# Kernel tuning notes

Hardware: AMD Instinct MI355X
Metric: run time of the kernel (lower is better)

## Reference

```python
import jax, jax.numpy as jnp
import numpy as np

N = 100_000      # num_nodes
E = 1_600_000    # num_edges (avg degree 16)
D = 64           # embedding_dim
L = 3            # num_layers


def setup_inputs() -> dict:
    key = jax.random.key(0)
    k1, k2 = jax.random.split(key)
    edge_index = jax.random.randint(k1, (2, E), 0, N, dtype=jnp.int64)
    edge_weight = jnp.ones((E,), jnp.float32)
    # nn.init.normal_(std=0.1)
    embedding = 0.1 * jax.random.normal(k2, (N, D), dtype=jnp.float32)
    return {"embedding": embedding, "edge_weight": edge_weight, "edge_index": edge_index}


def reference(embedding, edge_weight, edge_index):
    n = embedding.shape[0]
    self_idx = jnp.arange(n, dtype=edge_index.dtype)
    # add_self_loops: append (i, i) with weight 1 (PyG default fill_value)
    row = jnp.concatenate([edge_index[0], self_idx])  # source j
    col = jnp.concatenate([edge_index[1], self_idx])  # target i
    ew = jnp.concatenate([edge_weight, jnp.ones((n,), embedding.dtype)])
    # degree() counts occurrences of row (unweighted)
    deg = jax.ops.segment_sum(jnp.ones_like(ew), row, num_segments=n)
    deg_inv_sqrt = jnp.where(deg > 0, jax.lax.rsqrt(deg), 0.0)
    norm = deg_inv_sqrt[row] * ew * deg_inv_sqrt[col]  # [E+N]

    x = embedding
    acc = embedding  # running sum of layer-0..L embeddings
    for _ in range(L):
        # gather from source, scale, scatter-add to target (dropout off in eval)
        msg = norm[:, None] * x[row]                       # [E+N, D]
        x = jax.ops.segment_sum(msg, col, num_segments=n)  # [N, D]
        acc = acc + x
    return acc / (L + 1)
```

## Files before the change

### kernel.cpp

```cpp
#include <hip/hip_runtime.h>
#include <stdint.h>

#define DIM 64
#define BINS2 50000
#define RANGES 2
#define NSLICE 64
#define TBH 1024
#define SCAN_TILE 1024

__device__ __forceinline__ unsigned bf16rne(float f) {
    unsigned u = __float_as_uint(f);
    return (u + 0x7FFFu + ((u >> 16) & 1u)) >> 16;
}
__device__ __forceinline__ unsigned pack2(float lo, float hi) {
    return bf16rne(lo) | (bf16rne(hi) << 16);
}
#define UNPK(u, lo, hi) { lo = __uint_as_float((u) << 16); hi = __uint_as_float((u) & 0xFFFF0000u); }

__global__ void __launch_bounds__(TBH)
hist_kernel(const int* __restrict__ src, const int* __restrict__ dst,
            unsigned short* __restrict__ partialsA, unsigned short* __restrict__ partialsB,
            unsigned short* __restrict__ lrank, int E, int N, int Es) {
    __shared__ unsigned h32[BINS2 / 2];
    const int b = blockIdx.x;
    const int kind = b / (RANGES * NSLICE);
    const int rs = b % (RANGES * NSLICE);
    const int r = rs / NSLICE, s = rs % NSLICE;
    const int base = r * BINS2;
    const int hi = min(base + BINS2, N);
    const int nbw = (hi - base + 1) >> 1;
    for (int j = threadIdx.x; j < nbw; j += TBH) h32[j] = 0;
    __syncthreads();
    const int e0 = s * Es, e1 = min(e0 + Es, E);
    if (kind == 0) {
#pragma unroll 4
        for (int i = e0 + threadIdx.x; i < e1; i += TBH) {
            unsigned j = (unsigned)(dst[i] - base);
            if (j < (unsigned)BINS2) {
                const unsigned sh = (j & 1) * 16;
                unsigned old = atomicAdd(&h32[j >> 1], 1u << sh);
                lrank[i] = (unsigned short)((old >> sh) & 0xFFFFu);
            }
        }
    } else {
#pragma unroll 4
        for (int i = e0 + threadIdx.x; i < e1; i += TBH) {
            unsigned j = (unsigned)(src[i] - base);
            if (j < (unsigned)BINS2) atomicAdd(&h32[j >> 1], 1u << ((j & 1) * 16));
        }
    }
    __syncthreads();
    unsigned* part = (unsigned*)((kind ? partialsB : partialsA) + (size_t)s * N + base);
    for (int j = threadIdx.x; j < nbw; j += TBH) part[j] = h32[j];
}

__global__ void __launch_bounds__(256)
merge_kernel(unsigned short* __restrict__ partialsA, const unsigned short* __restrict__ partialsB,
             int* __restrict__ indeg, float* __restrict__ dis, int N) {
    const int i = blockIdx.x * blockDim.x + threadIdx.x;
    if (i >= N) return;
    int run = 0;
    for (int s = 0; s < NSLICE; ++s) {
        int v = partialsA[(size_t)s * N + i];
        partialsA[(size_t)s * N + i] = (unsigned short)run;
        run += v;
    }
    indeg[i] = run;
    int od = 0;
    for (int s = 0; s < NSLICE; ++s) od += partialsB[(size_t)s * N + i];
    dis[i] = rsqrtf((float)od + 1.0f);
}


__global__ void __launch_bounds__(256)
scan_partial(const int* __restrict__ indeg, int* __restrict__ partial, int n) {
    __shared__ int wsum[4];
    const int tid = threadIdx.x;
    const int base = blockIdx.x * SCAN_TILE + tid * 4;
    int s = 0;
    if (base + 3 < n) {
        int4 v = *(const int4*)(indeg + base);
        s = v.x + v.y + v.z + v.w;
    } else {
        for (int i = 0; i < 4; ++i) if (base + i < n) s += indeg[base + i];
    }
    for (int off = 32; off > 0; off >>= 1) s += __shfl_down(s, off, 64);
    const int lane = tid & 63, wid = tid >> 6;
    if (lane == 0) wsum[wid] = s;
    __syncthreads();
    if (tid == 0) partial[blockIdx.x] = wsum[0] + wsum[1] + wsum[2] + wsum[3];
}

__global__ void scan_blocksums(int* __restrict__ partial, int* __restrict__ offsets,
                               int nblocks, int n) {
    __shared__ int buf[1024];
    const int t = threadIdx.x;
    int v = (t < nblocks) ? partial[t] : 0;
    buf[t] = v;
    __syncthreads();
    for (int off = 1; off < 1024; off <<= 1) {
        int add = (t >= off) ? buf[t - off] : 0;
        __syncthreads();
        buf[t] += add;
        __syncthreads();
    }
    if (t < nblocks) partial[t] = buf[t] - v;
    if (t == 1023) offsets[n] = buf[1023];
}

__global__ void __launch_bounds__(256)
scan_final(const int* __restrict__ indeg, const int* __restrict__ partial,
           int* __restrict__ offsets, int n) {
    __shared__ int wpre[4];
    const int tid = threadIdx.x;
    const int base = blockIdx.x * SCAN_TILE + tid * 4;
    int v0 = 0, v1 = 0, v2 = 0, v3 = 0;
    if (base + 3 < n) {
        int4 v = *(const int4*)(indeg + base);
        v0 = v.x; v1 = v.y; v2 = v.z; v3 = v.w;
    } else {
        if (base + 0 < n) v0 = indeg[base + 0];
        if (base + 1 < n) v1 = indeg[base + 1];
        if (base + 2 < n) v2 = indeg[base + 2];
        if (base + 3 < n) v3 = indeg[base + 3];
    }
    const int s = v0 + v1 + v2 + v3;
    int inc = s;
    const int lane = tid & 63, wid = tid >> 6;
    for (int off = 1; off < 64; off <<= 1) {
        int t = __shfl_up(inc, off, 64);
        if (lane >= off) inc += t;
    }
    if (lane == 63) wpre[wid] = inc;
    __syncthreads();
    if (tid == 0) {
        int r = 0;
        for (int w = 0; w < 4; ++w) { int t = wpre[w]; wpre[w] = r; r += t; }
    }
    __syncthreads();
    int run = (inc - s) + wpre[wid] + partial[blockIdx.x];
    if (base + 0 < n) { offsets[base + 0] = run; run += v0; }
    if (base + 1 < n) { offsets[base + 1] = run; run += v1; }
    if (base + 2 < n) { offsets[base + 2] = run; run += v2; }
    if (base + 3 < n) { offsets[base + 3] = run; run += v3; }
}

__global__ void __launch_bounds__(256)
fill_kernel(const int* __restrict__ src, const int* __restrict__ dst,
            const float* __restrict__ ew, const float* __restrict__ dis,
            const int* __restrict__ offsets, const unsigned short* __restrict__ sliceoff,
            const unsigned short* __restrict__ lrank, int2* __restrict__ csr,
            int E, int N, int Es) {
    const int i0 = (blockIdx.x * blockDim.x + threadIdx.x) * 4;
    if (i0 + 3 < E) {
        int4   ss = *(const int4*)(src + i0);
        int4   tt = *(const int4*)(dst + i0);
        float4 ww = *(const float4*)(ew + i0);
        ushort4 lr = *(const ushort4*)(lrank + i0);
#define DO(K, SF, TF, WF, LF) { int sE = (i0 + K) / Es; \
        int slot = offsets[TF] + sliceoff[(size_t)sE * N + TF] + (int)(LF); \
        csr[slot] = make_int2(SF, __float_as_int(dis[SF] * (WF) * dis[TF])); }
        DO(0, ss.x, tt.x, ww.x, lr.x)
        DO(1, ss.y, tt.y, ww.y, lr.y)
        DO(2, ss.z, tt.z, ww.z, lr.z)
        DO(3, ss.w, tt.w, ww.w, lr.w)
#undef DO
    } else {
        for (int i = i0; i < E; ++i) {
            int sE = i / Es;
            int t = dst[i], sc = src[i];
            float w = dis[sc] * ew[i] * dis[t];
            int slot = offsets[t] + sliceoff[(size_t)sE * N + t] + (int)lrank[i];
            csr[slot] = make_int2(sc, __float_as_int(w));
        }
    }
}

__global__ void __launch_bounds__(256)
conv_kernel(const float4* __restrict__ in4, uint4* __restrict__ outb, int n8) {
    int i = blockIdx.x * blockDim.x + threadIdx.x;
    if (i >= n8) return;
    float4 a = in4[2 * i], b = in4[2 * i + 1];
    uint4 o;
    o.x = pack2(a.x, a.y); o.y = pack2(a.z, a.w);
    o.z = pack2(b.x, b.y); o.w = pack2(b.z, b.w);
    outb[i] = o;
}

__global__ void __launch_bounds__(256)
prop_kernel(const uint4* __restrict__ xg, const float4* __restrict__ selfF,
            uint4* __restrict__ xstore,
            const int* __restrict__ offsets, const int2* __restrict__ csr,
            const float* __restrict__ dis, int n) {
    const int lane = threadIdx.x & 63;
    const int fl  = lane & 7;
    const int sub = lane >> 3;
    const int wave = blockIdx.x * (blockDim.x >> 6) + (threadIdx.x >> 6);
    const int node = wave * 8 + sub;
    if (node >= n) return;

    const int beg = offsets[node];
    const int end = offsets[node + 1];
    const float d = dis[node];
    const float dd = d * d;

    float a0, a1, a2, a3, a4, a5, a6, a7;
    if (selfF) {
        float4 s0 = selfF[node * 16 + fl * 2];
        float4 s1 = selfF[node * 16 + fl * 2 + 1];
        a0 = dd * s0.x; a1 = dd * s0.y; a2 = dd * s0.z; a3 = dd * s0.w;
        a4 = dd * s1.x; a5 = dd * s1.y; a6 = dd * s1.z; a7 = dd * s1.w;
    } else {
        uint4 q = xg[(size_t)node * 8 + fl];
        float l, h;
        UNPK(q.x, l, h) a0 = dd * l; a1 = dd * h;
        UNPK(q.y, l, h) a2 = dd * l; a3 = dd * h;
        UNPK(q.z, l, h) a4 = dd * l; a5 = dd * h;
        UNPK(q.w, l, h) a6 = dd * l; a7 = dd * h;
    }

#define EDGE(E, Q) { float w_ = __int_as_float((E).y); float l, h; \
    UNPK((Q).x, l, h) a0 = fmaf(w_, l, a0); a1 = fmaf(w_, h, a1); \
    UNPK((Q).y, l, h) a2 = fmaf(w_, l, a2); a3 = fmaf(w_, h, a3); \
    UNPK((Q).z, l, h) a4 = fmaf(w_, l, a4); a5 = fmaf(w_, h, a5); \
    UNPK((Q).w, l, h) a6 = fmaf(w_, l, a6); a7 = fmaf(w_, h, a7); }

    int p = beg;
    for (; p + 8 <= end; p += 8) {
        int2 e0 = csr[p + 0], e1 = csr[p + 1], e2 = csr[p + 2], e3 = csr[p + 3];
        int2 e4 = csr[p + 4], e5 = csr[p + 5], e6 = csr[p + 6], e7 = csr[p + 7];
        uint4 q0 = xg[(size_t)e0.x * 8 + fl];
        uint4 q1 = xg[(size_t)e1.x * 8 + fl];
        uint4 q2 = xg[(size_t)e2.x * 8 + fl];
        uint4 q3 = xg[(size_t)e3.x * 8 + fl];
        uint4 q4 = xg[(size_t)e4.x * 8 + fl];
        uint4 q5 = xg[(size_t)e5.x * 8 + fl];
        uint4 q6 = xg[(size_t)e6.x * 8 + fl];
        uint4 q7 = xg[(size_t)e7.x * 8 + fl];
        EDGE(e0, q0) EDGE(e1, q1) EDGE(e2, q2) EDGE(e3, q3)
        EDGE(e4, q4) EDGE(e5, q5) EDGE(e6, q6) EDGE(e7, q7)
    }
    for (; p + 4 <= end; p += 4) {
        int2 e0 = csr[p + 0], e1 = csr[p + 1], e2 = csr[p + 2], e3 = csr[p + 3];
        uint4 q0 = xg[(size_t)e0.x * 8 + fl];
        uint4 q1 = xg[(size_t)e1.x * 8 + fl];
        uint4 q2 = xg[(size_t)e2.x * 8 + fl];
        uint4 q3 = xg[(size_t)e3.x * 8 + fl];
        EDGE(e0, q0) EDGE(e1, q1) EDGE(e2, q2) EDGE(e3, q3)
    }
    for (; p < end; ++p) {
        int2 e = csr[p];
        uint4 q = xg[(size_t)e.x * 8 + fl];
        EDGE(e, q)
    }
#undef EDGE

    uint4 o;
    o.x = pack2(a0, a1); o.y = pack2(a2, a3);
    o.z = pack2(a4, a5); o.w = pack2(a6, a7);
    xstore[(size_t)node * 8 + fl] = o;
}

__global__ void __launch_bounds__(256)
combine_kernel(const float4* __restrict__ emb4, const uint4* __restrict__ xa,
               const uint4* __restrict__ xb, const uint4* __restrict__ xc,
               float4* __restrict__ out4, int n8) {
    int i = blockIdx.x * blockDim.x + threadIdx.x;
    if (i >= n8) return;
    float4 e0 = emb4[2 * i], e1 = emb4[2 * i + 1];
    uint4 qa = xa[i], qb = xb[i], qc = xc[i];
    float r[8] = { e0.x, e0.y, e0.z, e0.w, e1.x, e1.y, e1.z, e1.w };
    float l, h;
    UNPK(qa.x, l, h) r[0] += l; r[1] += h;
    UNPK(qa.y, l, h) r[2] += l; r[3] += h;
    UNPK(qa.z, l, h) r[4] += l; r[5] += h;
    UNPK(qa.w, l, h) r[6] += l; r[7] += h;
    UNPK(qb.x, l, h) r[0] += l; r[1] += h;
    UNPK(qb.y, l, h) r[2] += l; r[3] += h;
    UNPK(qb.z, l, h) r[4] += l; r[5] += h;
    UNPK(qb.w, l, h) r[6] += l; r[7] += h;
    UNPK(qc.x, l, h) r[0] += l; r[1] += h;
    UNPK(qc.y, l, h) r[2] += l; r[3] += h;
    UNPK(qc.z, l, h) r[4] += l; r[5] += h;
    UNPK(qc.w, l, h) r[6] += l; r[7] += h;
    out4[2 * i]     = make_float4(0.25f * r[0], 0.25f * r[1], 0.25f * r[2], 0.25f * r[3]);
    out4[2 * i + 1] = make_float4(0.25f * r[4], 0.25f * r[5], 0.25f * r[6], 0.25f * r[7]);
}


extern "C" void kernel_launch(void* const* d_in, const int* in_sizes, int n_in,
                              void* d_out, int out_size, void* d_ws, size_t ws_size,
                              hipStream_t stream) {
    const float* emb = (const float*)d_in[0];
    const float* ew  = (const float*)d_in[1];
    const int*   ei  = (const int*)d_in[2];
    const int E = in_sizes[2] / 2;
    const int N = in_sizes[0] / DIM;
    const int* src = ei;
    const int* dst = ei + E;
    float* out = (float*)d_out;

    const int Es = (E + NSLICE - 1) / NSLICE;
    const int nscan = (N + SCAN_TILE - 1) / SCAN_TILE;

    char* w = (char*)d_ws;
    size_t partSz = ((size_t)NSLICE * N * 2 + 255) & ~(size_t)255;
    size_t xSz    = ((size_t)N * DIM * 2 + 255) & ~(size_t)255;
    size_t uSz    = (partSz > xSz) ? partSz : xSz;
    unsigned short* partialsA = (unsigned short*)w;
    uint4* xc = (uint4*)w; w += uSz;
    unsigned short* partialsB = (unsigned short*)w;
    uint4* xb = (uint4*)w; w += uSz;
    unsigned short* lrank = (unsigned short*)w; w += (size_t)E * 2;
    int* indeg   = (int*)w;  w += (size_t)N * 4;
    int* offsets = (int*)w;  w += (size_t)(N + 1) * 4;
    float* dis   = (float*)w; w += (size_t)N * 4;
    int* partial = (int*)w;  w += (size_t)1024 * 4;
    w = (char*)(((uintptr_t)w + 255) & ~(uintptr_t)255);
    int2* csr    = (int2*)w; w += (size_t)E * 8;
    w = (char*)(((uintptr_t)w + 255) & ~(uintptr_t)255);
    uint4* x0c   = (uint4*)w; w += xSz;
    uint4* xa    = (uint4*)w; w += xSz;

    const int TB = 256;
    hist_kernel<<<2 * RANGES * NSLICE, TBH, 0, stream>>>(src, dst, partialsA, partialsB,
                                                         lrank, E, N, Es);
    merge_kernel<<<(N + TB - 1) / TB, TB, 0, stream>>>(partialsA, partialsB,
                                                       indeg, dis, N);
    scan_partial<<<nscan, TB, 0, stream>>>(indeg, partial, N);
    scan_blocksums<<<1, 1024, 0, stream>>>(partial, offsets, nscan, N);
    scan_final<<<nscan, TB, 0, stream>>>(indeg, partial, offsets, N);
    const int e4 = (E + 3) / 4;
    fill_kernel<<<(e4 + TB - 1) / TB, TB, 0, stream>>>(src, dst, ew, dis, offsets,
                                                       partialsA, lrank, csr, E, N, Es);
    const int n8 = N * DIM / 8;
    conv_kernel<<<(n8 + TB - 1) / TB, TB, 0, stream>>>((const float4*)emb, x0c, n8);

    dim3 grid((N + 31) / 32), block(TB);
    prop_kernel<<<grid, block, 0, stream>>>(x0c, (const float4*)emb, xa,
                                            offsets, csr, dis, N);
    prop_kernel<<<grid, block, 0, stream>>>(xa, nullptr, xb,
                                            offsets, csr, dis, N);
    prop_kernel<<<grid, block, 0, stream>>>(xb, nullptr, xc,
                                            offsets, csr, dis, N);
    combine_kernel<<<(n8 + TB - 1) / TB, TB, 0, stream>>>((const float4*)emb, xa, xb, xc,
                                                          (float4*)out, n8);
}
```

Before: 284.8 us.

## Replace sliced shared-memory histogram CSR build with global atomics and two-pass bucketed placement

Replaces the 64-slice shared-memory histogram plus per-slice prefix merge with global-atomic degree counting. The CSR is now built by partitioning edges into 128-node buckets via block-local histograms and global cursors, then placing them within each bucket using shared-memory atomics. The aim is to avoid the large NSLICE×N partial arrays and the scattered per-edge slot writes. The cost is an extra staging pass over E records, contended global atomics, and an in-bucket edge order that is no longer deterministic. That order changes the floating-point summation order, and the source index must fit in 20 bits.

```diff
diff --git a/kernel.cpp b/kernel.cpp
--- a/kernel.cpp
+++ b/kernel.cpp
@@ -2,10 +2,10 @@
 #include <stdint.h>
 
 #define DIM 64
-#define BINS2 50000
-#define RANGES 2
-#define NSLICE 64
-#define TBH 1024
+#define GB 128
+#define GSH 7
+#define CH 8192
+#define TB1 512
 #define SCAN_TILE 1024
 
 __device__ __forceinline__ unsigned bf16rne(float f) {
@@ -17,58 +17,23 @@
 }
 #define UNPK(u, lo, hi) { lo = __uint_as_float((u) << 16); hi = __uint_as_float((u) & 0xFFFF0000u); }
 
-__global__ void __launch_bounds__(TBH)
-hist_kernel(const int* __restrict__ src, const int* __restrict__ dst,
-            unsigned short* __restrict__ partialsA, unsigned short* __restrict__ partialsB,
-            unsigned short* __restrict__ lrank, int E, int N, int Es) {
-    __shared__ unsigned h32[BINS2 / 2];
-    const int b = blockIdx.x;
-    const int kind = b / (RANGES * NSLICE);
-    const int rs = b % (RANGES * NSLICE);
-    const int r = rs / NSLICE, s = rs % NSLICE;
-    const int base = r * BINS2;
-    const int hi = min(base + BINS2, N);
-    const int nbw = (hi - base + 1) >> 1;
-    for (int j = threadIdx.x; j < nbw; j += TBH) h32[j] = 0;
-    __syncthreads();
-    const int e0 = s * Es, e1 = min(e0 + Es, E);
-    if (kind == 0) {
-#pragma unroll 4
-        for (int i = e0 + threadIdx.x; i < e1; i += TBH) {
-            unsigned j = (unsigned)(dst[i] - base);
-            if (j < (unsigned)BINS2) {
-                const unsigned sh = (j & 1) * 16;
-                unsigned old = atomicAdd(&h32[j >> 1], 1u << sh);
-                lrank[i] = (unsigned short)((old >> sh) & 0xFFFFu);
-            }
+__global__ void __launch_bounds__(256)
+deg_kernel(const int* __restrict__ src, const int* __restrict__ dst,
+           int* __restrict__ indeg, int* __restrict__ outdeg, int E) {
+    const int i0 = (blockIdx.x * blockDim.x + threadIdx.x) * 4;
+    if (i0 + 3 < E) {
+        int4 ss = *(const int4*)(src + i0);
+        int4 tt = *(const int4*)(dst + i0);
+        atomicAdd(&outdeg[ss.x], 1); atomicAdd(&outdeg[ss.y], 1);
+        atomicAdd(&outdeg[ss.z], 1); atomicAdd(&outdeg[ss.w], 1);
+        atomicAdd(&indeg[tt.x], 1);  atomicAdd(&indeg[tt.y], 1);
+        atomicAdd(&indeg[tt.z], 1);  atomicAdd(&indeg[tt.w], 1);
+    } else {
+        for (int i = i0; i < E; ++i) {
+            atomicAdd(&outdeg[src[i]], 1);
+            atomicAdd(&indeg[dst[i]], 1);
         }
-    } else {
-#pragma unroll 4
-        for (int i = e0 + threadIdx.x; i < e1; i += TBH) {
-            unsigned j = (unsigned)(src[i] - base);
-            if (j < (unsigned)BINS2) atomicAdd(&h32[j >> 1], 1u << ((j & 1) * 16));
-        }
-    }
-    __syncthreads();
-    unsigned* part = (unsigned*)((kind ? partialsB : partialsA) + (size_t)s * N + base);
-    for (int j = threadIdx.x; j < nbw; j += TBH) part[j] = h32[j];
-}
-
-__global__ void __launch_bounds__(256)
-merge_kernel(unsigned short* __restrict__ partialsA, const unsigned short* __restrict__ partialsB,
-             int* __restrict__ indeg, float* __restrict__ dis, int N) {
-    const int i = blockIdx.x * blockDim.x + threadIdx.x;
-    if (i >= N) return;
-    int run = 0;
-    for (int s = 0; s < NSLICE; ++s) {
-        int v = partialsA[(size_t)s * N + i];
-        partialsA[(size_t)s * N + i] = (unsigned short)run;
-        run += v;
-    }
-    indeg[i] = run;
-    int od = 0;
-    for (int s = 0; s < NSLICE; ++s) od += partialsB[(size_t)s * N + i];
-    dis[i] = rsqrtf((float)od + 1.0f);
+    }
 }
 
 
@@ -146,33 +111,87 @@
 }
 
 __global__ void __launch_bounds__(256)
-fill_kernel(const int* __restrict__ src, const int* __restrict__ dst,
+prep_kernel(const int* __restrict__ outdeg, const int* __restrict__ offsets,
+            float* __restrict__ dis, int* __restrict__ cursor, int N, int NB) {
+    const int i = blockIdx.x * blockDim.x + threadIdx.x;
+    if (i < N) dis[i] = rsqrtf((float)outdeg[i] + 1.0f);
+    if (i < NB) cursor[i] = offsets[i << GSH];
+}
+
+__global__ void __launch_bounds__(TB1)
+part_kernel(const int* __restrict__ src, const int* __restrict__ dst,
             const float* __restrict__ ew, const float* __restrict__ dis,
-            const int* __restrict__ offsets, const unsigned short* __restrict__ sliceoff,
-            const unsigned short* __restrict__ lrank, int2* __restrict__ csr,
-            int E, int N, int Es) {
-    const int i0 = (blockIdx.x * blockDim.x + threadIdx.x) * 4;
-    if (i0 + 3 < E) {
-        int4   ss = *(const int4*)(src + i0);
-        int4   tt = *(const int4*)(dst + i0);
-        float4 ww = *(const float4*)(ew + i0);
-        ushort4 lr = *(const ushort4*)(lrank + i0);
-#define DO(K, SF, TF, WF, LF) { int sE = (i0 + K) / Es; \
-        int slot = offsets[TF] + sliceoff[(size_t)sE * N + TF] + (int)(LF); \
-        csr[slot] = make_int2(SF, __float_as_int(dis[SF] * (WF) * dis[TF])); }
-        DO(0, ss.x, tt.x, ww.x, lr.x)
-        DO(1, ss.y, tt.y, ww.y, lr.y)
-        DO(2, ss.z, tt.z, ww.z, lr.z)
-        DO(3, ss.w, tt.w, ww.w, lr.w)
-#undef DO
-    } else {
-        for (int i = i0; i < E; ++i) {
-            int sE = i / Es;
-            int t = dst[i], sc = src[i];
-            float w = dis[sc] * ew[i] * dis[t];
-            int slot = offsets[t] + sliceoff[(size_t)sE * N + t] + (int)lrank[i];
-            csr[slot] = make_int2(sc, __float_as_int(w));
+            int* __restrict__ cursor, int2* __restrict__ staged, int E, int NB) {
+    __shared__ int h[1024];
+    const int tid = threadIdx.x;
+    const int e0 = blockIdx.x * CH;
+    const int e1 = min(e0 + CH, E);
+    for (int j = tid; j < NB; j += TB1) h[j] = 0;
+    __syncthreads();
+    int4 d[4];
+    int ngrp = 0;
+    for (int i = e0 + tid * 4, k = 0; i < e1; i += TB1 * 4, ++k) {
+        int4 t;
+        if (i + 3 < e1) t = *(const int4*)(dst + i);
+        else {
+            t.x = dst[i];
+            t.y = (i + 1 < e1) ? dst[i + 1] : -1;
+            t.z = (i + 2 < e1) ? dst[i + 2] : -1;
+            t.w = (i + 3 < e1) ? dst[i + 3] : -1;
         }
+        d[k] = t;
+        if (t.x >= 0) atomicAdd(&h[t.x >> GSH], 1);
+        if (t.y >= 0) atomicAdd(&h[t.y >> GSH], 1);
+        if (t.z >= 0) atomicAdd(&h[t.z >> GSH], 1);
+        if (t.w >= 0) atomicAdd(&h[t.w >> GSH], 1);
+        ngrp = k + 1;
+    }
+    __syncthreads();
+    for (int j = tid; j < NB; j += TB1) {
+        int c = h[j];
+        h[j] = c ? atomicAdd(&cursor[j], c) : 0;
+    }
+    __syncthreads();
+    for (int i = e0 + tid * 4, k = 0; k < ngrp; i += TB1 * 4, ++k) {
+        int4 t = d[k];
+        int4 ss = make_int4(0, 0, 0, 0);
+        float4 ww = make_float4(0.f, 0.f, 0.f, 0.f);
+        if (i + 3 < e1) { ss = *(const int4*)(src + i); ww = *(const float4*)(ew + i); }
+        else {
+            ss.x = src[i]; ww.x = ew[i];
+            if (i + 1 < e1) { ss.y = src[i + 1]; ww.y = ew[i + 1]; }
+            if (i + 2 < e1) { ss.z = src[i + 2]; ww.z = ew[i + 2]; }
+            if (i + 3 < e1) { ss.w = src[i + 3]; ww.w = ew[i + 3]; }
+        }
+#define PART1(T, S, W) if ((T) >= 0) { \
+        float w_ = dis[S] * (W) * dis[T]; \
+        int pos_ = atomicAdd(&h[(T) >> GSH], 1); \
+        staged[pos_] = make_int2((S) | (((T) & (GB - 1)) << 20), __float_as_int(w_)); }
+        PART1(t.x, ss.x, ww.x)
+        PART1(t.y, ss.y, ww.y)
+        PART1(t.z, ss.z, ww.z)
+        PART1(t.w, ss.w, ww.w)
+#undef PART1
+    }
+}
+
+__global__ void __launch_bounds__(256)
+place_kernel(const int2* __restrict__ staged, const int* __restrict__ offsets,
+             int2* __restrict__ csr, int N) {
+    __shared__ int offs[GB + 1];
+    __shared__ int cnt[GB];
+    const int n0 = blockIdx.x << GSH;
+    const int nb = min(GB, N - n0);
+    for (int j = threadIdx.x; j < nb + 1; j += 256) offs[j] = offsets[n0 + j];
+    for (int j = threadIdx.x; j < GB; j += 256) cnt[j] = 0;
+    __syncthreads();
+    const int r0 = offs[0], r1 = offs[nb];
+    for (int i = r0 + threadIdx.x; i < r1; i += 256) {
+        int2 rec = staged[i];
+        int tl = (rec.x >> 20) & (GB - 1);
+        int s = rec.x & 0xFFFFF;
+        int rank = atomicAdd(&cnt[tl], 1);
+        csr[offs[tl] + rank] = make_int2(s, rec.y);
     }
 }
 
@@ -300,39 +319,39 @@
     const int* dst = ei + E;
     float* out = (float*)d_out;
 
-    const int Es = (E + NSLICE - 1) / NSLICE;
+    const int NB = (N + GB - 1) >> GSH;
     const int nscan = (N + SCAN_TILE - 1) / SCAN_TILE;
 
     char* w = (char*)d_ws;
-    size_t partSz = ((size_t)NSLICE * N * 2 + 255) & ~(size_t)255;
-    size_t xSz    = ((size_t)N * DIM * 2 + 255) & ~(size_t)255;
-    size_t uSz    = (partSz > xSz) ? partSz : xSz;
-    unsigned short* partialsA = (unsigned short*)w;
-    uint4* xc = (uint4*)w; w += uSz;
-    unsigned short* partialsB = (unsigned short*)w;
-    uint4* xb = (uint4*)w; w += uSz;
-    unsigned short* lrank = (unsigned short*)w; w += (size_t)E * 2;
-    int* indeg   = (int*)w;  w += (size_t)N * 4;
-    int* offsets = (int*)w;  w += (size_t)(N + 1) * 4;
-    float* dis   = (float*)w; w += (size_t)N * 4;
-    int* partial = (int*)w;  w += (size_t)1024 * 4;
-    w = (char*)(((uintptr_t)w + 255) & ~(uintptr_t)255);
-    int2* csr    = (int2*)w; w += (size_t)E * 8;
-    w = (char*)(((uintptr_t)w + 255) & ~(uintptr_t)255);
+    size_t xSz = ((size_t)N * DIM * 2 + 255) & ~(size_t)255;
+    size_t sSz = ((size_t)E * 8 + 255) & ~(size_t)255;
+    size_t uSz = (sSz > xSz) ? sSz : xSz;
+    int2* staged = (int2*)w;
+    uint4* xb    = (uint4*)w; w += uSz;
+    int2* csr    = (int2*)w; w += sSz;
     uint4* x0c   = (uint4*)w; w += xSz;
     uint4* xa    = (uint4*)w; w += xSz;
+    uint4* xc    = (uint4*)w; w += xSz;
+    int* indeg   = (int*)w; int* outdeg = indeg + N;
+    w += ((size_t)2 * N * 4 + 255) & ~(size_t)255;
+    int* offsets = (int*)w; w += ((size_t)(N + 1) * 4 + 255) & ~(size_t)255;
+    float* dis   = (float*)w; w += ((size_t)N * 4 + 255) & ~(size_t)255;
+    int* partial = (int*)w; w += 4096;
+    int* cursor  = (int*)w; w += ((size_t)NB * 4 + 255) & ~(size_t)255;
 
     const int TB = 256;
-    hist_kernel<<<2 * RANGES * NSLICE, TBH, 0, stream>>>(src, dst, partialsA, partialsB,
-                                                         lrank, E, N, Es);
-    merge_kernel<<<(N + TB - 1) / TB, TB, 0, stream>>>(partialsA, partialsB,
-                                                       indeg, dis, N);
+    hipMemsetAsync(indeg, 0, (size_t)2 * N * 4, stream);
+
+    const int e4 = (E + 3) / 4;
+    deg_kernel<<<(e4 + TB - 1) / TB, TB, 0, stream>>>(src, dst, indeg, outdeg, E);
     scan_partial<<<nscan, TB, 0, stream>>>(indeg, partial, N);
     scan_blocksums<<<1, 1024, 0, stream>>>(partial, offsets, nscan, N);
     scan_final<<<nscan, TB, 0, stream>>>(indeg, partial, offsets, N);
-    const int e4 = (E + 3) / 4;
-    fill_kernel<<<(e4 + TB - 1) / TB, TB, 0, stream>>>(src, dst, ew, dis, offsets,
-                                                       partialsA, lrank, csr, E, N, Es);
+    prep_kernel<<<(N + TB - 1) / TB, TB, 0, stream>>>(outdeg, offsets, dis, cursor, N, NB);
+    part_kernel<<<(E + CH - 1) / CH, TB1, 0, stream>>>(src, dst, ew, dis, cursor,
+                                                       staged, E, NB);
+    place_kernel<<<NB, TB, 0, stream>>>(staged, offsets, csr, N);
+
     const int n8 = N * DIM / 8;
     conv_kernel<<<(n8 + TB - 1) / TB, TB, 0, stream>>>((const float4*)emb, x0c, n8);
 
```

After: 381.6 us. 1.34x slower.
